# Performance work log

Measured on AMD Instinct MI355X. Metric: run time of the kernel, lower is better.

## Reference

```python
import jax, jax.numpy as jnp
import numpy as np

FP8_E4M3_MAX = 448.0
BLOCK = 32
EPS = 1e-30


def _quantize_fp8(blocks):
    # blocks: (..., num_blocks, BLOCK) float32
    max_abs = jnp.max(jnp.abs(blocks), axis=-1)                      # (..., nb)
    scales = jnp.maximum(max_abs / FP8_E4M3_MAX, EPS)                # shared fp32 scale per block
    fp8 = (blocks / scales[..., None]).astype(jnp.float8_e4m3fn).astype(jnp.float32)
    return fp8, scales


def setup_inputs() -> dict:
    key = jax.random.key(0)
    k1, k2, k3 = jax.random.split(key, 3)
    x = jax.random.normal(k1, (2048, 2048), dtype=jnp.float32)
    weight = jax.random.normal(k2, (2048, 2048), dtype=jnp.float32) * 0.02
    bias = jax.random.normal(k3, (2048,), dtype=jnp.float32) * 0.02
    return {"x": x, "weight": weight, "bias": bias}


def reference(x, weight, bias):
    N, in_f = x.shape
    out_f = weight.shape[0]
    nb = in_f // BLOCK  # in_features is a multiple of BLOCK, so no padding needed

    x_fp8, x_scales = _quantize_fp8(x.reshape(N, nb, BLOCK))         # (N, nb, B), (N, nb)
    w_fp8, w_scales = _quantize_fp8(weight.reshape(out_f, nb, BLOCK))  # (out, nb, B), (out, nb)

    # per-block fp8-element dot products: (nb, N, out)
    elem_dots = jnp.einsum('nbk,jbk->bnj', x_fp8, w_fp8)
    # apply shared block scales and reduce over blocks: out[n,j] = sum_b sx[n,b]*sw[j,b]*dots[b,n,j]
    result = jnp.einsum('bnj,nb,jb->nj', elem_dots, x_scales, w_scales)
    return result + bias
```

## Files before the change

### kernel.cpp

```cpp
#include <hip/hip_runtime.h>
#include <hip/hip_bf16.h>


typedef __attribute__((ext_vector_type(8))) __bf16 bf16x8;
typedef __attribute__((ext_vector_type(4))) float f32x4;

#define NMAT 2048
#define FP8_MAX 448.0f

__device__ inline unsigned short bfbits(float f) {
  union { __hip_bfloat16 h; unsigned short u; } cv;
  cv.h = __float2bfloat16(f);
  return cv.u;
}

__device__ inline unsigned pack2(float a, float b, float scale) {
  int p = __builtin_amdgcn_cvt_pk_fp8_f32(a / scale, b / scale, 0, false);
  float qa = __builtin_amdgcn_cvt_f32_fp8(p, 0) * scale;
  float qb = __builtin_amdgcn_cvt_f32_fp8(p, 1) * scale;
  return (unsigned)bfbits(qa) | ((unsigned)bfbits(qb) << 16);
}

__global__ __launch_bounds__(256) void qdq_kernel(const float* __restrict__ x,
                                                  uint2* __restrict__ xo,
                                                  const float* __restrict__ w,
                                                  uint2* __restrict__ wo) {
  int g = blockIdx.x;
  const float* in;
  uint2* out;
  if (g >= 4096) { in = w; out = wo; g -= 4096; }
  else           { in = x; out = xo; }
  const int t = threadIdx.x;
  const size_t base = (size_t)g * 1024;
  float4 v = ((const float4*)(in + base))[t];
  float amax = fmaxf(fmaxf(fabsf(v.x), fabsf(v.y)), fmaxf(fabsf(v.z), fabsf(v.w)));
  amax = fmaxf(amax, __shfl_xor(amax, 1));
  amax = fmaxf(amax, __shfl_xor(amax, 2));
  amax = fmaxf(amax, __shfl_xor(amax, 4));
  float scale = fmaxf(amax / FP8_MAX, 1e-30f);
  uint2 r;
  r.x = pack2(v.x, v.y, scale);
  r.y = pack2(v.z, v.w, scale);
  out[base / 4 + t] = r;
}

__global__ __launch_bounds__(256) void gemm_kernel(const __bf16* __restrict__ A,
                                                   const __bf16* __restrict__ B,
                                                   const float* __restrict__ bias,
                                                   float* __restrict__ C) {
  __shared__ __align__(16) char lds[49152];
  const int tid  = threadIdx.x;
  const int lane = tid & 63;
  const int wid  = tid >> 6;
  const int wr   = wid >> 1;
  const int wc   = wid & 1;
  const int row0 = blockIdx.y * 128;
  const int col0 = blockIdx.x * 64;

  int rS[4], cS[4];
#pragma unroll
  for (int i = 0; i < 4; ++i) {
    const int o = i * 4096 + tid * 16;
    rS[i] = o >> 7;
    cS[i] = (o & 127) ^ ((rS[i] & 7) << 4);
  }
  const char* AgS[4];
  const char* BgS[2];
#pragma unroll
  for (int i = 0; i < 4; ++i)
    AgS[i] = (const char*)A + (size_t)(row0 + rS[i]) * 4096 + cS[i];
#pragma unroll
  for (int j = 0; j < 2; ++j)
    BgS[j] = (const char*)B + (size_t)(col0 + rS[j]) * 4096 + cS[j];
  const int dst = tid * 16;

#define STAGE(buf, kt) do {                                                      \
    const int kb = (kt) * 128;                                                   \
    char* lb = lds + (buf) * 24576;                                              \
    _Pragma("unroll")                                                            \
    for (int i = 0; i < 4; ++i)                                                  \
      __builtin_amdgcn_global_load_lds(                                          \
          (const __attribute__((address_space(1))) unsigned*)(AgS[i] + kb),      \
          (__attribute__((address_space(3))) unsigned*)(lb + i * 4096 + dst),    \
          16, 0, 0);                                                             \
    _Pragma("unroll")                                                            \
    for (int j = 0; j < 2; ++j)                                                  \
      __builtin_amdgcn_global_load_lds(                                          \
          (const __attribute__((address_space(1))) unsigned*)(BgS[j] + kb),      \
          (__attribute__((address_space(3))) unsigned*)(lb + 16384 + j * 4096 + dst), \
          16, 0, 0);                                                             \
  } while (0)

  const int l15 = lane & 15;
  const int q16 = (lane >> 4) * 16;
  const int swz = (l15 & 7) << 4;
  const int ck0 = q16 ^ swz;
  const int ck1 = (64 + q16) ^ swz;
  const int aRow = (wr * 64 + l15) * 128;
  const int bRow = (wc * 32 + l15) * 128;

  f32x4 acc[4][2] = {};

  auto compute = [&](const int buf) {
    const char* ab = lds + buf * 24576;
    const char* bb = ab + 16384;
    bf16x8 a0[4], a1[4], b0[2], b1[2];
#pragma unroll
    for (int m = 0; m < 4; ++m) {
      a0[m] = *(const bf16x8*)(ab + aRow + m * 2048 + ck0);
      a1[m] = *(const bf16x8*)(ab + aRow + m * 2048 + ck1);
    }
#pragma unroll
    for (int n = 0; n < 2; ++n) {
      b0[n] = *(const bf16x8*)(bb + bRow + n * 2048 + ck0);
      b1[n] = *(const bf16x8*)(bb + bRow + n * 2048 + ck1);
    }
#pragma unroll
    for (int m = 0; m < 4; ++m)
#pragma unroll
      for (int n = 0; n < 2; ++n) {
        acc[m][n] = __builtin_amdgcn_mfma_f32_16x16x32_bf16(a0[m], b0[n], acc[m][n], 0, 0, 0);
        acc[m][n] = __builtin_amdgcn_mfma_f32_16x16x32_bf16(a1[m], b1[n], acc[m][n], 0, 0, 0);
      }
  };

  STAGE(0, 0);
  __syncthreads();
#pragma unroll 1
  for (int t = 0; t < 30; t += 2) {
    STAGE(1, t + 1);
    compute(0);
    __syncthreads();
    STAGE(0, t + 2);
    compute(1);
    __syncthreads();
  }
  STAGE(1, 31);
  compute(0);
  __syncthreads();
  compute(1);

  const int rb = row0 + wr * 64 + (lane >> 4) * 4;
#pragma unroll
  for (int n = 0; n < 2; ++n) {
    const int j = col0 + wc * 32 + n * 16 + l15;
    const float bv = bias[j];
#pragma unroll
    for (int m = 0; m < 4; ++m)
#pragma unroll
      for (int r = 0; r < 4; ++r)
        C[(size_t)(rb + m * 16 + r) * NMAT + j] = acc[m][n][r] + bv;
  }
#undef STAGE
}

extern "C" void kernel_launch(void* const* d_in, const int* in_sizes, int n_in,
                              void* d_out, int out_size, void* d_ws, size_t ws_size,
                              hipStream_t stream) {
  const float* x  = (const float*)d_in[0];
  const float* w  = (const float*)d_in[1];
  const float* bs = (const float*)d_in[2];
  float* out = (float*)d_out;

  uint2* xd = (uint2*)d_ws;
  uint2* wd = xd + (NMAT * (size_t)NMAT / 4);

  qdq_kernel<<<dim3(8192), dim3(256), 0, stream>>>(x, xd, w, wd);

  dim3 grid(NMAT / 64, NMAT / 128);
  gemm_kernel<<<grid, dim3(256), 0, stream>>>((const __bf16*)xd, (const __bf16*)wd,
                                              bs, out);
}
```

Before: 105.5 us.

## Triple-buffer GEMM with 2-wave blocks, larger per-wave tiles and grid swizzle

Reworks the bf16 GEMM to use 128-thread blocks where each wave computes a 64x64 tile instead of 64x32, and adds a third LDS buffer. Partial vmcnt waits with raw barriers let two K-tiles stay in flight while one is computed. A 1D grid with a block-index swizzle is meant to improve L2 reuse. The aim is to hide global-to-LDS latency and raise MFMA density per LDS read, at the cost of fewer waves per block, more registers and 72KB of LDS, which may limit occupancy.

```diff
diff --git a/kernel.cpp b/kernel.cpp
--- a/kernel.cpp
+++ b/kernel.cpp
@@ -44,106 +44,120 @@
   out[base / 4 + t] = r;
 }
 
-__global__ __launch_bounds__(256) void gemm_kernel(const __bf16* __restrict__ A,
-                                                   const __bf16* __restrict__ B,
-                                                   const float* __restrict__ bias,
-                                                   float* __restrict__ C) {
-  __shared__ __align__(16) char lds[49152];
+__global__ __launch_bounds__(128, 1) void gemm_kernel(const __bf16* __restrict__ A,
+                                                      const __bf16* __restrict__ B,
+                                                      const float* __restrict__ bias,
+                                                      float* __restrict__ C) {
+  __shared__ __align__(16) char lds[73728];
   const int tid  = threadIdx.x;
   const int lane = tid & 63;
   const int wid  = tid >> 6;
-  const int wr   = wid >> 1;
-  const int wc   = wid & 1;
-  const int row0 = blockIdx.y * 128;
-  const int col0 = blockIdx.x * 64;
 
-  int rS[4], cS[4];
+  const int bid = blockIdx.x;
+  const int swz = (bid & 7) * 64 + (bid >> 3);
+  const int row0 = (swz >> 5) * 128;
+  const int col0 = (swz & 31) * 64;
+
+  const char* AgS[8];
+  const char* BgS[4];
 #pragma unroll
-  for (int i = 0; i < 4; ++i) {
-    const int o = i * 4096 + tid * 16;
-    rS[i] = o >> 7;
-    cS[i] = (o & 127) ^ ((rS[i] & 7) << 4);
+  for (int i = 0; i < 8; ++i) {
+    const int o = i * 2048 + tid * 16;
+    const int r = o >> 7;
+    const int c = (o & 127) ^ ((r & 7) << 4);
+    AgS[i] = (const char*)A + (size_t)(row0 + r) * 4096 + c;
+    if (i < 4)
+      BgS[i] = (const char*)B + (size_t)(col0 + r) * 4096 + c;
   }
-  const char* AgS[4];
-  const char* BgS[2];
-#pragma unroll
-  for (int i = 0; i < 4; ++i)
-    AgS[i] = (const char*)A + (size_t)(row0 + rS[i]) * 4096 + cS[i];
-#pragma unroll
-  for (int j = 0; j < 2; ++j)
-    BgS[j] = (const char*)B + (size_t)(col0 + rS[j]) * 4096 + cS[j];
   const int dst = tid * 16;
 
 #define STAGE(buf, kt) do {                                                      \
     const int kb = (kt) * 128;                                                   \
     char* lb = lds + (buf) * 24576;                                              \
     _Pragma("unroll")                                                            \
-    for (int i = 0; i < 4; ++i)                                                  \
+    for (int i = 0; i < 8; ++i)                                                  \
       __builtin_amdgcn_global_load_lds(                                          \
           (const __attribute__((address_space(1))) unsigned*)(AgS[i] + kb),      \
-          (__attribute__((address_space(3))) unsigned*)(lb + i * 4096 + dst),    \
+          (__attribute__((address_space(3))) unsigned*)(lb + i * 2048 + dst),    \
           16, 0, 0);                                                             \
     _Pragma("unroll")                                                            \
-    for (int j = 0; j < 2; ++j)                                                  \
+    for (int j = 0; j < 4; ++j)                                                  \
       __builtin_amdgcn_global_load_lds(                                          \
           (const __attribute__((address_space(1))) unsigned*)(BgS[j] + kb),      \
-          (__attribute__((address_space(3))) unsigned*)(lb + 16384 + j * 4096 + dst), \
+          (__attribute__((address_space(3))) unsigned*)(lb + 16384 + j * 2048 + dst), \
           16, 0, 0);                                                             \
+  } while (0)
+
+#define WAITBAR(N) do {                                            \
+    asm volatile("s_waitcnt vmcnt(" #N ")" ::: "memory");          \
+    __builtin_amdgcn_sched_barrier(0);                             \
+    __builtin_amdgcn_s_barrier();                                  \
+  } while (0)
+#define PBAR() do {                                                \
+    __builtin_amdgcn_sched_barrier(0);                             \
+    __builtin_amdgcn_s_barrier();                                  \
   } while (0)
 
   const int l15 = lane & 15;
   const int q16 = (lane >> 4) * 16;
-  const int swz = (l15 & 7) << 4;
-  const int ck0 = q16 ^ swz;
-  const int ck1 = (64 + q16) ^ swz;
-  const int aRow = (wr * 64 + l15) * 128;
-  const int bRow = (wc * 32 + l15) * 128;
+  const int swb = (l15 & 7) << 4;
+  const int ck0 = q16 ^ swb;
+  const int ck1 = (64 + q16) ^ swb;
+  const int aRow = (wid * 64 + l15) * 128;
+  const int bRow = l15 * 128;
 
-  f32x4 acc[4][2] = {};
+  f32x4 acc[4][4] = {};
 
   auto compute = [&](const int buf) {
     const char* ab = lds + buf * 24576;
     const char* bb = ab + 16384;
-    bf16x8 a0[4], a1[4], b0[2], b1[2];
+    bf16x8 a0[4], a1[4], b0[4], b1[4];
 #pragma unroll
     for (int m = 0; m < 4; ++m) {
       a0[m] = *(const bf16x8*)(ab + aRow + m * 2048 + ck0);
       a1[m] = *(const bf16x8*)(ab + aRow + m * 2048 + ck1);
     }
 #pragma unroll
-    for (int n = 0; n < 2; ++n) {
+    for (int n = 0; n < 4; ++n) {
       b0[n] = *(const bf16x8*)(bb + bRow + n * 2048 + ck0);
       b1[n] = *(const bf16x8*)(bb + bRow + n * 2048 + ck1);
     }
 #pragma unroll
     for (int m = 0; m < 4; ++m)
 #pragma unroll
-      for (int n = 0; n < 2; ++n) {
+      for (int n = 0; n < 4; ++n) {
         acc[m][n] = __builtin_amdgcn_mfma_f32_16x16x32_bf16(a0[m], b0[n], acc[m][n], 0, 0, 0);
         acc[m][n] = __builtin_amdgcn_mfma_f32_16x16x32_bf16(a1[m], b1[n], acc[m][n], 0, 0, 0);
       }
   };
 
   STAGE(0, 0);
-  __syncthreads();
+  STAGE(1, 1);
 #pragma unroll 1
-  for (int t = 0; t < 30; t += 2) {
-    STAGE(1, t + 1);
+  for (int t = 0; t < 30; t += 3) {
+    STAGE(2, t + 2);
+    WAITBAR(24);
     compute(0);
-    __syncthreads();
-    STAGE(0, t + 2);
+    PBAR();
+    STAGE(0, t + 3);
+    WAITBAR(24);
     compute(1);
-    __syncthreads();
+    PBAR();
+    STAGE(1, t + 4);
+    WAITBAR(24);
+    compute(2);
+    PBAR();
   }
-  STAGE(1, 31);
+  WAITBAR(12);
   compute(0);
-  __syncthreads();
+  PBAR();
+  WAITBAR(0);
   compute(1);
 
-  const int rb = row0 + wr * 64 + (lane >> 4) * 4;
+  const int rb = row0 + wid * 64 + (lane >> 4) * 4;
 #pragma unroll
-  for (int n = 0; n < 2; ++n) {
-    const int j = col0 + wc * 32 + n * 16 + l15;
+  for (int n = 0; n < 4; ++n) {
+    const int j = col0 + n * 16 + l15;
     const float bv = bias[j];
 #pragma unroll
     for (int m = 0; m < 4; ++m)
@@ -152,6 +166,8 @@
         C[(size_t)(rb + m * 16 + r) * NMAT + j] = acc[m][n][r] + bv;
   }
 #undef STAGE
+#undef WAITBAR
+#undef PBAR
 }
 
 extern "C" void kernel_launch(void* const* d_in, const int* in_sizes, int n_in,
@@ -167,7 +183,6 @@
 
   qdq_kernel<<<dim3(8192), dim3(256), 0, stream>>>(x, xd, w, wd);
 
-  dim3 grid(NMAT / 64, NMAT / 128);
-  gemm_kernel<<<grid, dim3(256), 0, stream>>>((const __bf16*)xd, (const __bf16*)wd,
-                                              bs, out);
+  gemm_kernel<<<dim3(512), dim3(128), 0, stream>>>((const __bf16*)xd,
+                                                   (const __bf16*)wd, bs, out);
 }
```

New measurement: 104.1 us. Within noise of the previous version (-1.3%).
